# Performance work log

Measured on AMD Instinct MI355X. Metric: run time of the kernel, lower is better.

Reference implementation:

```python
import jax, jax.numpy as jnp
import numpy as np

N_NODES = 100000
N_EDGES = 1600000
D_FEAT = 128
HIDDEN = 128
N_CLASSES = 10
NUM_GRAPHS = 64


def setup_inputs() -> dict:
    key = jax.random.key(0)
    ks = jax.random.split(key, 12)
    x = jax.random.normal(ks[0], (N_NODES, D_FEAT), dtype=jnp.float32)
    edge_index = jax.random.randint(ks[1], (2, N_EDGES), 0, N_NODES, dtype=jnp.int32)
    batch = jnp.sort(jax.random.randint(ks[2], (N_NODES,), 0, NUM_GRAPHS, dtype=jnp.int32))
    s = 1.0 / np.sqrt(HIDDEN)
    def lin(k, out_d, in_d):
        return jax.random.uniform(k, (out_d, in_d), jnp.float32, -s, s)
    return {
        "x": x,
        "edge_index": edge_index,
        "batch": batch,
        "W1l": lin(ks[3], HIDDEN, D_FEAT), "b1": jnp.zeros((HIDDEN,), jnp.float32),
        "W1r": lin(ks[4], HIDDEN, D_FEAT),
        "W2l": lin(ks[5], HIDDEN, HIDDEN), "b2": jnp.zeros((HIDDEN,), jnp.float32),
        "W2r": lin(ks[6], HIDDEN, HIDDEN),
        "W3l": lin(ks[7], HIDDEN, HIDDEN), "b3": jnp.zeros((HIDDEN,), jnp.float32),
        "W3r": lin(ks[8], HIDDEN, HIDDEN),
        "Wout": lin(ks[9], N_CLASSES, HIDDEN), "bout": jnp.zeros((N_CLASSES,), jnp.float32),
    }


def reference(x, edge_index, batch, W1l, b1, W1r, W2l, b2, W2r, W3l, b3, W3r, Wout, bout):
    src, dst = edge_index[0], edge_index[1]
    n = x.shape[0]

    def sage(h, Wl, b, Wr):
        # sum-aggregate neighbor features: scatter-add x[src] into dst rows
        agg = jax.ops.segment_sum(h[src], dst, num_segments=n)  # [N, d]
        return agg @ Wl.T + b + h @ Wr.T

    h = jax.nn.relu(sage(x, W1l, b1, W1r))
    h = jax.nn.relu(sage(h, W2l, b2, W2r))
    h = sage(h, W3l, b3, W3r)
    pooled = jax.ops.segment_sum(h, batch, num_segments=NUM_GRAPHS)  # [G, hidden]
    # dropout is identity in eval mode
    return pooled @ Wout.T + bout
```

## Files before the change

kernel.cpp:

```cpp
#include <hip/hip_runtime.h>
#include <hip/hip_bf16.h>

#define N_NODES  100000
#define N_EDGES  1600000
#define D_FEAT   128
#define HIDDEN   128
#define N_CLASSES 10
#define NUM_GRAPHS 64

#define NBUCK 250
#define NPB   400
#define BCAP  7168
#define GT    64
#define NPAD  100096
#define NTILES (NPAD / GT)

typedef __bf16 bf16x8 __attribute__((ext_vector_type(8)));
typedef float  f32x4  __attribute__((ext_vector_type(4)));

static __device__ __forceinline__ unsigned short f2bf(float f) {
    __bf16 b = (__bf16)f;
    return __builtin_bit_cast(unsigned short, b);
}

static __device__ __forceinline__ void async_copy16(void* lds, const void* g) {
    __builtin_amdgcn_global_load_lds(
        (const __attribute__((address_space(1))) void*)g,
        (__attribute__((address_space(3))) void*)lds, 16, 0, 0);
}

__global__ void conv_w6_kernel(const float* __restrict__ W0, const float* __restrict__ W1,
                               const float* __restrict__ W2, const float* __restrict__ W3,
                               const float* __restrict__ W4, const float* __restrict__ W5,
                               __bf16* __restrict__ out) {
    const float* Ws[6] = {W0, W1, W2, W3, W4, W5};
    int m = blockIdx.x >> 6;
    int i = (blockIdx.x & 63) * 256 + threadIdx.x;
    out[m * (HIDDEN * D_FEAT) + i] = (__bf16)Ws[m][i];
}

__global__ __launch_bounds__(256) void xconv_kernel(const float* __restrict__ x,
                                                    __bf16* __restrict__ out) {
    int i = blockIdx.x * 256 + threadIdx.x;
    bf16x8 o;
    if (i < N_NODES * 128 / 8) {
        float4 v0 = ((const float4*)x)[i * 2];
        float4 v1 = ((const float4*)x)[i * 2 + 1];
        o[0] = (__bf16)v0.x; o[1] = (__bf16)v0.y; o[2] = (__bf16)v0.z; o[3] = (__bf16)v0.w;
        o[4] = (__bf16)v1.x; o[5] = (__bf16)v1.y; o[6] = (__bf16)v1.z; o[7] = (__bf16)v1.w;
    } else {
        #pragma unroll
        for (int k = 0; k < 8; k++) o[k] = (__bf16)0.f;
    }
    if (i < NPAD * 128 / 8) ((bf16x8*)out)[i] = o;
}

__global__ __launch_bounds__(256) void bucket_scatter_kernel(const int* __restrict__ ei,
                                                             int* __restrict__ gcur,
                                                             int2* __restrict__ bkt) {
    __shared__ int h[NBUCK];
    __shared__ int lb[NBUCK];
    int t = threadIdx.x;
    const int CH = N_EDGES / 256;
    for (int i = t; i < NBUCK; i += 256) h[i] = 0;
    __syncthreads();
    int e0 = blockIdx.x * CH;
    for (int e = e0 + t; e < e0 + CH; e += 256) {
        int d = ei[N_EDGES + e];
        atomicAdd(&h[d / NPB], 1);
    }
    __syncthreads();
    for (int i = t; i < NBUCK; i += 256) {
        lb[i] = atomicAdd(&gcur[i], h[i]);
        h[i] = 0;
    }
    __syncthreads();
    for (int e = e0 + t; e < e0 + CH; e += 256) {
        int s = ei[e];
        int d = ei[N_EDGES + e];
        int bb = d / NPB;
        int pos = lb[bb] + atomicAdd(&h[bb], 1);
        if (pos < BCAP) bkt[(size_t)bb * BCAP + pos] = make_int2(s, d);
    }
}

__global__ __launch_bounds__(256) void bucket_csr_kernel(const int2* __restrict__ bkt,
                                                         const int* __restrict__ gcur,
                                                         int2* __restrict__ rpse,
                                                         int* __restrict__ csr_src) {
    const int b = blockIdx.x;
    const int n0 = b * NPB;
    const int base = b * BCAP;
    int m = gcur[b]; if (m > BCAP) m = BCAP;
    __shared__ int cnt[NPB];
    __shared__ int part[128];
    __shared__ int excl[NPB];
    int t = threadIdx.x;
    for (int i = t; i < NPB; i += 256) cnt[i] = 0;
    __syncthreads();
    for (int e = t; e < m; e += 256) {
        int2 p = bkt[base + e];
        atomicAdd(&cnt[p.y - n0], 1);
    }
    __syncthreads();
    int gs = 0;
    if (t < 100) { gs = cnt[4 * t] + cnt[4 * t + 1] + cnt[4 * t + 2] + cnt[4 * t + 3]; part[t] = gs; }
    else if (t < 128) part[t] = 0;
    __syncthreads();
    for (int off = 1; off < 128; off <<= 1) {
        int x = 0;
        if (t < 128 && t >= off) x = part[t - off];
        __syncthreads();
        if (t < 128) part[t] += x;
        __syncthreads();
    }
    if (t < 100) part[t] -= gs;
    __syncthreads();
    for (int i = t; i < NPB; i += 256) {
        int g = i >> 2;
        int e0 = part[g];
        for (int j = g * 4; j < i; j++) e0 += cnt[j];
        excl[i] = e0;
    }
    __syncthreads();
    for (int i = t; i < NPB; i += 256) {
        rpse[n0 + i] = make_int2(base + excl[i], base + excl[i] + cnt[i]);
    }
    __syncthreads();
    for (int i = t; i < NPB; i += 256) cnt[i] = excl[i];
    __syncthreads();
    for (int e = t; e < m; e += 256) {
        int2 p = bkt[base + e];
        int pos = base + atomicAdd(&cnt[p.y - n0], 1);
        csr_src[pos] = p.x;
    }
}

__global__ __launch_bounds__(256) void gather_kernel(
    const __bf16* __restrict__ h, const int2* __restrict__ rpse,
    const int* __restrict__ csr_src, __bf16* __restrict__ agg, int N)
{
    int nid = blockIdx.x * 16 + (threadIdx.x >> 4);
    if (nid >= N) return;
    int f8 = threadIdx.x & 15;
    int2 se = rpse[nid];

    float a[8] = {0.f, 0.f, 0.f, 0.f, 0.f, 0.f, 0.f, 0.f};

    int j = se.x;
    for (; j + 3 < se.y; j += 4) {
        int s0 = csr_src[j];
        int s1 = csr_src[j + 1];
        int s2 = csr_src[j + 2];
        int s3 = csr_src[j + 3];
        bf16x8 u0 = ((const bf16x8*)h)[(size_t)s0 * 16 + f8];
        bf16x8 u1 = ((const bf16x8*)h)[(size_t)s1 * 16 + f8];
        bf16x8 u2 = ((const bf16x8*)h)[(size_t)s2 * 16 + f8];
        bf16x8 u3 = ((const bf16x8*)h)[(size_t)s3 * 16 + f8];
        #pragma unroll
        for (int i = 0; i < 8; i++)
            a[i] += ((float)u0[i] + (float)u1[i]) + ((float)u2[i] + (float)u3[i]);
    }
    for (; j < se.y; j++) {
        int s0 = csr_src[j];
        bf16x8 u0 = ((const bf16x8*)h)[(size_t)s0 * 16 + f8];
        #pragma unroll
        for (int i = 0; i < 8; i++) a[i] += (float)u0[i];
    }
    bf16x8 o;
    #pragma unroll
    for (int i = 0; i < 8; i++) o[i] = (__bf16)a[i];
    ((bf16x8*)agg)[(size_t)nid * 16 + f8] = o;
}

template<bool RELU>
__global__ __launch_bounds__(256) void fused_gemm_kernel(
    const __bf16* __restrict__ hA,
    const __bf16* __restrict__ hG,
    const __bf16* __restrict__ Wl, const __bf16* __restrict__ Wr,
    const float* __restrict__ bias,
    __bf16* __restrict__ outp, int M)
{
    __shared__ __bf16 lds[2][GT * 128];

    const int tid  = threadIdx.x;
    const int wave = tid >> 6;
    const int lane = tid & 63;
    const int kq = lane >> 4;
    const int ln = lane & 15;
    const int node_base = blockIdx.x * GT;
    const int f_base = wave * 32;

    {
        const __bf16* gsrc = hG + (size_t)node_base * 128;
        const __bf16* asrc = hA + (size_t)node_base * 128;
        #pragma unroll
        for (int i = 0; i < 4; i++) {
            int u = i * 256 + tid;
            int row = u >> 4;
            int sc = (u & 15) ^ (row & 15);
            async_copy16(&lds[0][u * 8], gsrc + row * 128 + sc * 8);
            async_copy16(&lds[1][u * 8], asrc + row * 128 + sc * 8);
        }
    }

    bf16x8 wfragL[2][4], wfragR[2][4];
    #pragma unroll
    for (int t = 0; t < 2; t++) {
        int wrow = f_base + t * 16 + ln;
        #pragma unroll
        for (int kc = 0; kc < 4; kc++) {
            int k0 = kc * 32 + kq * 8;
            wfragL[t][kc] = *(const bf16x8*)(Wl + wrow * 128 + k0);
            wfragR[t][kc] = *(const bf16x8*)(Wr + wrow * 128 + k0);
        }
    }
    float4 bias4[2];
    bias4[0] = *(const float4*)(bias + f_base + kq * 4);
    bias4[1] = *(const float4*)(bias + f_base + 16 + kq * 4);

    __syncthreads();

    #pragma unroll 2
    for (int tau = 0; tau < GT / 16; tau++) {
        int r = tau * 16 + ln;
        bf16x8 gfrag[4], afrag[4];
        #pragma unroll
        for (int kc = 0; kc < 4; kc++) {
            int c = (4 * kc + kq) ^ ln;
            gfrag[kc] = *(const bf16x8*)&lds[0][r * 128 + c * 8];
            afrag[kc] = *(const bf16x8*)&lds[1][r * 128 + c * 8];
        }

        f32x4 acc[2] = {(f32x4)(0.f), (f32x4)(0.f)};
        #pragma unroll
        for (int kc = 0; kc < 4; kc++) {
            #pragma unroll
            for (int t = 0; t < 2; t++) {
                acc[t] = __builtin_amdgcn_mfma_f32_16x16x32_bf16(wfragL[t][kc], gfrag[kc], acc[t], 0, 0, 0);
                acc[t] = __builtin_amdgcn_mfma_f32_16x16x32_bf16(wfragR[t][kc], afrag[kc], acc[t], 0, 0, 0);
            }
        }

        int node = node_base + tau * 16 + ln;
        if (node < M) {
            size_t rowoff = (size_t)node * 128;
            #pragma unroll
            for (int t = 0; t < 2; t++) {
                int fc = f_base + t * 16 + kq * 4;
                ushort4 o;
                float v0 = acc[t][0] + bias4[t].x;
                float v1 = acc[t][1] + bias4[t].y;
                float v2 = acc[t][2] + bias4[t].z;
                float v3 = acc[t][3] + bias4[t].w;
                if (RELU) {
                    v0 = fmaxf(v0, 0.f); v1 = fmaxf(v1, 0.f);
                    v2 = fmaxf(v2, 0.f); v3 = fmaxf(v3, 0.f);
                }
                o.x = f2bf(v0); o.y = f2bf(v1); o.z = f2bf(v2); o.w = f2bf(v3);
                *(ushort4*)(outp + rowoff + fc) = o;
            }
        }
    }
}

__global__ __launch_bounds__(256) void pool_kernel(
    const __bf16* __restrict__ h, const int* __restrict__ batch,
    float* __restrict__ pooled, int N)
{
    int idx = blockIdx.x * 256 + threadIdx.x;
    int f = idx & 127;
    int chunk = idx >> 7;
    int n0 = chunk * 32;
    if (n0 >= N) return;
    int n1 = n0 + 32; if (n1 > N) n1 = N;
    int curb = batch[n0];
    float acc = 0.f;
    for (int n = n0; n < n1; n++) {
        int b = batch[n];
        if (b != curb) {
            unsafeAtomicAdd(&pooled[(size_t)curb * 128 + f], acc);
            acc = 0.f; curb = b;
        }
        acc += (float)h[(size_t)n * 128 + f];
    }
    unsafeAtomicAdd(&pooled[(size_t)curb * 128 + f], acc);
}

__global__ void final_gemm_kernel(
    const float* __restrict__ pooled, const float* __restrict__ Wout,
    const float* __restrict__ bout, float* __restrict__ out)
{
    int idx = blockIdx.x * 64 + threadIdx.x;
    if (idx < NUM_GRAPHS * N_CLASSES) {
        int g = idx / N_CLASSES;
        int c = idx % N_CLASSES;
        float acc = bout[c];
        for (int k = 0; k < HIDDEN; k++)
            acc += pooled[g * HIDDEN + k] * Wout[c * HIDDEN + k];
        out[idx] = acc;
    }
}

extern "C" void kernel_launch(void* const* d_in, const int* in_sizes, int n_in,
                              void* d_out, int out_size, void* d_ws, size_t ws_size,
                              hipStream_t stream) {
    const float* x     = (const float*)d_in[0];
    const int*   ei    = (const int*)d_in[1];
    const int*   batch = (const int*)d_in[2];
    const float* W1l = (const float*)d_in[3];
    const float* b1  = (const float*)d_in[4];
    const float* W1r = (const float*)d_in[5];
    const float* W2l = (const float*)d_in[6];
    const float* b2  = (const float*)d_in[7];
    const float* W2r = (const float*)d_in[8];
    const float* W3l = (const float*)d_in[9];
    const float* b3  = (const float*)d_in[10];
    const float* W3r = (const float*)d_in[11];
    const float* Wout = (const float*)d_in[12];
    const float* bout = (const float*)d_in[13];
    float* out = (float*)d_out;

    char* ws = (char*)d_ws;
    size_t off = 0;
    const size_t NB = (size_t)NPAD * 128 * sizeof(__bf16);
    __bf16* B0    = (__bf16*)(ws + off); off += NB;
    __bf16* B1    = (__bf16*)(ws + off); off += NB;
    __bf16* B2    = (__bf16*)(ws + off); off += NB;
    float* pooled = (float*)(ws + off);  off += (size_t)NUM_GRAPHS * HIDDEN * sizeof(float);
    __bf16* wbf   = (__bf16*)(ws + off); off += 6 * (size_t)HIDDEN * D_FEAT * sizeof(__bf16);
    int2* rpse    = (int2*)(ws + off);   off += (size_t)N_NODES * sizeof(int2);
    int* csr_src  = (int*)(ws + off);    off += (size_t)NBUCK * BCAP * sizeof(int);
    int2* bkt     = (int2*)(ws + off);   off += (size_t)NBUCK * BCAP * sizeof(int2);
    int* gcur     = (int*)(ws + off);    off += (NBUCK + 8) * sizeof(int);

    const int WSZ = HIDDEN * D_FEAT;

    conv_w6_kernel<<<6 * 64, 256, 0, stream>>>(W1l, W1r, W2l, W2r, W3l, W3r, wbf);
    xconv_kernel<<<NPAD * 128 / (256 * 8), 256, 0, stream>>>(x, B0);

    hipMemsetAsync(gcur, 0, NBUCK * sizeof(int), stream);
    bucket_scatter_kernel<<<256, 256, 0, stream>>>(ei, gcur, bkt);
    bucket_csr_kernel<<<NBUCK, 256, 0, stream>>>(bkt, gcur, rpse, csr_src);

    const int gath_grid = (N_NODES + 15) / 16;

    gather_kernel<<<gath_grid, 256, 0, stream>>>(B0, rpse, csr_src, B1, N_NODES);
    fused_gemm_kernel<true><<<NTILES, 256, 0, stream>>>(B0, B1, wbf + 0 * WSZ, wbf + 1 * WSZ, b1, B2, N_NODES);

    gather_kernel<<<gath_grid, 256, 0, stream>>>(B2, rpse, csr_src, B1, N_NODES);
    fused_gemm_kernel<true><<<NTILES, 256, 0, stream>>>(B2, B1, wbf + 2 * WSZ, wbf + 3 * WSZ, b2, B0, N_NODES);

    gather_kernel<<<gath_grid, 256, 0, stream>>>(B0, rpse, csr_src, B1, N_NODES);
    fused_gemm_kernel<false><<<NTILES, 256, 0, stream>>>(B0, B1, wbf + 4 * WSZ, wbf + 5 * WSZ, b3, B2, N_NODES);

    hipMemsetAsync(pooled, 0, (size_t)NUM_GRAPHS * HIDDEN * sizeof(float), stream);
    const int pool_grid = ((N_NODES + 31) / 32 * 128 + 255) / 256;
    pool_kernel<<<pool_grid, 256, 0, stream>>>(B2, batch, pooled, N_NODES);
    final_gemm_kernel<<<10, 64, 0, stream>>>(pooled, Wout, bout, out);
}
```

Measured before the change: 439.7 us.

## Fuse last-layer GEMM with pooling, pack bucket entries, widen gather batching

```diff
diff --git a/kernel.cpp b/kernel.cpp
--- a/kernel.cpp
+++ b/kernel.cpp
@@ -57,11 +57,11 @@
 
 __global__ __launch_bounds__(256) void bucket_scatter_kernel(const int* __restrict__ ei,
                                                              int* __restrict__ gcur,
-                                                             int2* __restrict__ bkt) {
+                                                             int* __restrict__ bkt) {
     __shared__ int h[NBUCK];
     __shared__ int lb[NBUCK];
     int t = threadIdx.x;
-    const int CH = N_EDGES / 256;
+    const int CH = N_EDGES / 64;
     for (int i = t; i < NBUCK; i += 256) h[i] = 0;
     __syncthreads();
     int e0 = blockIdx.x * CH;
@@ -80,11 +80,11 @@
         int d = ei[N_EDGES + e];
         int bb = d / NPB;
         int pos = lb[bb] + atomicAdd(&h[bb], 1);
-        if (pos < BCAP) bkt[(size_t)bb * BCAP + pos] = make_int2(s, d);
-    }
-}
-
-__global__ __launch_bounds__(256) void bucket_csr_kernel(const int2* __restrict__ bkt,
+        if (pos < BCAP) bkt[(size_t)bb * BCAP + pos] = s | ((d - bb * NPB) << 17);
+    }
+}
+
+__global__ __launch_bounds__(256) void bucket_csr_kernel(const int* __restrict__ bkt,
                                                          const int* __restrict__ gcur,
                                                          int2* __restrict__ rpse,
                                                          int* __restrict__ csr_src) {
@@ -99,8 +99,8 @@
     for (int i = t; i < NPB; i += 256) cnt[i] = 0;
     __syncthreads();
     for (int e = t; e < m; e += 256) {
-        int2 p = bkt[base + e];
-        atomicAdd(&cnt[p.y - n0], 1);
+        int p = bkt[base + e];
+        atomicAdd(&cnt[p >> 17], 1);
     }
     __syncthreads();
     int gs = 0;
@@ -130,9 +130,9 @@
     for (int i = t; i < NPB; i += 256) cnt[i] = excl[i];
     __syncthreads();
     for (int e = t; e < m; e += 256) {
-        int2 p = bkt[base + e];
-        int pos = base + atomicAdd(&cnt[p.y - n0], 1);
-        csr_src[pos] = p.x;
+        int p = bkt[base + e];
+        int pos = base + atomicAdd(&cnt[p >> 17], 1);
+        csr_src[pos] = p & 131071;
     }
 }
 
@@ -144,28 +144,31 @@
     if (nid >= N) return;
     int f8 = threadIdx.x & 15;
     int2 se = rpse[nid];
+    int deg = se.y - se.x;
 
     float a[8] = {0.f, 0.f, 0.f, 0.f, 0.f, 0.f, 0.f, 0.f};
 
-    int j = se.x;
-    for (; j + 3 < se.y; j += 4) {
-        int s0 = csr_src[j];
-        int s1 = csr_src[j + 1];
-        int s2 = csr_src[j + 2];
-        int s3 = csr_src[j + 3];
-        bf16x8 u0 = ((const bf16x8*)h)[(size_t)s0 * 16 + f8];
-        bf16x8 u1 = ((const bf16x8*)h)[(size_t)s1 * 16 + f8];
-        bf16x8 u2 = ((const bf16x8*)h)[(size_t)s2 * 16 + f8];
-        bf16x8 u3 = ((const bf16x8*)h)[(size_t)s3 * 16 + f8];
-        #pragma unroll
-        for (int i = 0; i < 8; i++)
-            a[i] += ((float)u0[i] + (float)u1[i]) + ((float)u2[i] + (float)u3[i]);
-    }
-    for (; j < se.y; j++) {
-        int s0 = csr_src[j];
-        bf16x8 u0 = ((const bf16x8*)h)[(size_t)s0 * 16 + f8];
-        #pragma unroll
-        for (int i = 0; i < 8; i++) a[i] += (float)u0[i];
+    if (deg > 0) {
+        int iters = (deg + 7) >> 3;
+        int j = se.x;
+        #pragma unroll 1
+        for (int it = 0; it < iters; it++, j += 8) {
+            bf16x8 u[8];
+            float msk[8];
+            #pragma unroll
+            for (int i = 0; i < 8; i++) {
+                int jj = j + i;
+                int cl = jj < se.y ? jj : se.y - 1;
+                int s = csr_src[cl];
+                u[i] = ((const bf16x8*)h)[(size_t)s * 16 + f8];
+                msk[i] = (jj < se.y) ? 1.f : 0.f;
+            }
+            #pragma unroll
+            for (int i = 0; i < 8; i++) {
+                #pragma unroll
+                for (int k = 0; k < 8; k++) a[k] += msk[i] * (float)u[i][k];
+            }
+        }
     }
     bf16x8 o;
     #pragma unroll
@@ -175,8 +178,7 @@
 
 template<bool RELU>
 __global__ __launch_bounds__(256) void fused_gemm_kernel(
-    const __bf16* __restrict__ hA,
-    const __bf16* __restrict__ hG,
+    const __bf16* __restrict__ hA, const __bf16* __restrict__ hG,
     const __bf16* __restrict__ Wl, const __bf16* __restrict__ Wr,
     const float* __restrict__ bias,
     __bf16* __restrict__ outp, int M)
@@ -248,7 +250,6 @@
             #pragma unroll
             for (int t = 0; t < 2; t++) {
                 int fc = f_base + t * 16 + kq * 4;
-                ushort4 o;
                 float v0 = acc[t][0] + bias4[t].x;
                 float v1 = acc[t][1] + bias4[t].y;
                 float v2 = acc[t][2] + bias4[t].z;
@@ -257,6 +258,7 @@
                     v0 = fmaxf(v0, 0.f); v1 = fmaxf(v1, 0.f);
                     v2 = fmaxf(v2, 0.f); v3 = fmaxf(v3, 0.f);
                 }
+                ushort4 o;
                 o.x = f2bf(v0); o.y = f2bf(v1); o.z = f2bf(v2); o.w = f2bf(v3);
                 *(ushort4*)(outp + rowoff + fc) = o;
             }
@@ -264,27 +266,126 @@
     }
 }
 
-__global__ __launch_bounds__(256) void pool_kernel(
-    const __bf16* __restrict__ h, const int* __restrict__ batch,
-    float* __restrict__ pooled, int N)
+__global__ __launch_bounds__(256) void fused_gemm_pool_kernel(
+    const __bf16* __restrict__ hA, const __bf16* __restrict__ hG,
+    const __bf16* __restrict__ Wl, const __bf16* __restrict__ Wr,
+    const float* __restrict__ bias, const int* __restrict__ batch,
+    float* __restrict__ pooled, int M)
 {
-    int idx = blockIdx.x * 256 + threadIdx.x;
-    int f = idx & 127;
-    int chunk = idx >> 7;
-    int n0 = chunk * 32;
-    if (n0 >= N) return;
-    int n1 = n0 + 32; if (n1 > N) n1 = N;
-    int curb = batch[n0];
-    float acc = 0.f;
-    for (int n = n0; n < n1; n++) {
-        int b = batch[n];
-        if (b != curb) {
-            unsafeAtomicAdd(&pooled[(size_t)curb * 128 + f], acc);
-            acc = 0.f; curb = b;
-        }
-        acc += (float)h[(size_t)n * 128 + f];
-    }
-    unsafeAtomicAdd(&pooled[(size_t)curb * 128 + f], acc);
+    __shared__ __bf16 lds[2][GT * 128];
+
+    const int tid  = threadIdx.x;
+    const int wave = tid >> 6;
+    const int lane = tid & 63;
+    const int kq = lane >> 4;
+    const int ln = lane & 15;
+    const int node_base = blockIdx.x * GT;
+    const int f_base = wave * 32;
+
+    {
+        const __bf16* gsrc = hG + (size_t)node_base * 128;
+        const __bf16* asrc = hA + (size_t)node_base * 128;
+        #pragma unroll
+        for (int i = 0; i < 4; i++) {
+            int u = i * 256 + tid;
+            int row = u >> 4;
+            int sc = (u & 15) ^ (row & 15);
+            async_copy16(&lds[0][u * 8], gsrc + row * 128 + sc * 8);
+            async_copy16(&lds[1][u * 8], asrc + row * 128 + sc * 8);
+        }
+    }
+
+    bf16x8 wfragL[2][4], wfragR[2][4];
+    #pragma unroll
+    for (int t = 0; t < 2; t++) {
+        int wrow = f_base + t * 16 + ln;
+        #pragma unroll
+        for (int kc = 0; kc < 4; kc++) {
+            int k0 = kc * 32 + kq * 8;
+            wfragL[t][kc] = *(const bf16x8*)(Wl + wrow * 128 + k0);
+            wfragR[t][kc] = *(const bf16x8*)(Wr + wrow * 128 + k0);
+        }
+    }
+    float4 bias4[2];
+    bias4[0] = *(const float4*)(bias + f_base + kq * 4);
+    bias4[1] = *(const float4*)(bias + f_base + 16 + kq * 4);
+
+    int nb_cl = node_base < M ? node_base : (M - 1);
+    int ne_cl = node_base + GT - 1 < M ? node_base + GT - 1 : (M - 1);
+    int g0 = batch[nb_cl];
+    bool uniform = (batch[ne_cl] == g0) && (node_base + GT <= M);
+
+    float pacc[2][4] = {{0.f,0.f,0.f,0.f},{0.f,0.f,0.f,0.f}};
+
+    __syncthreads();
+
+    #pragma unroll 2
+    for (int tau = 0; tau < GT / 16; tau++) {
+        int r = tau * 16 + ln;
+        bf16x8 gfrag[4], afrag[4];
+        #pragma unroll
+        for (int kc = 0; kc < 4; kc++) {
+            int c = (4 * kc + kq) ^ ln;
+            gfrag[kc] = *(const bf16x8*)&lds[0][r * 128 + c * 8];
+            afrag[kc] = *(const bf16x8*)&lds[1][r * 128 + c * 8];
+        }
+
+        f32x4 acc[2] = {(f32x4)(0.f), (f32x4)(0.f)};
+        #pragma unroll
+        for (int kc = 0; kc < 4; kc++) {
+            #pragma unroll
+            for (int t = 0; t < 2; t++) {
+                acc[t] = __builtin_amdgcn_mfma_f32_16x16x32_bf16(wfragL[t][kc], gfrag[kc], acc[t], 0, 0, 0);
+                acc[t] = __builtin_amdgcn_mfma_f32_16x16x32_bf16(wfragR[t][kc], afrag[kc], acc[t], 0, 0, 0);
+            }
+        }
+
+        int node = node_base + tau * 16 + ln;
+        if (uniform) {
+            #pragma unroll
+            for (int t = 0; t < 2; t++) {
+                pacc[t][0] += acc[t][0] + bias4[t].x;
+                pacc[t][1] += acc[t][1] + bias4[t].y;
+                pacc[t][2] += acc[t][2] + bias4[t].z;
+                pacc[t][3] += acc[t][3] + bias4[t].w;
+            }
+        } else if (node < M) {
+            int g = batch[node];
+            #pragma unroll
+            for (int t = 0; t < 2; t++) {
+                int fc = f_base + t * 16 + kq * 4;
+                unsafeAtomicAdd(&pooled[g * 128 + fc + 0], acc[t][0] + bias4[t].x);
+                unsafeAtomicAdd(&pooled[g * 128 + fc + 1], acc[t][1] + bias4[t].y);
+                unsafeAtomicAdd(&pooled[g * 128 + fc + 2], acc[t][2] + bias4[t].z);
+                unsafeAtomicAdd(&pooled[g * 128 + fc + 3], acc[t][3] + bias4[t].w);
+            }
+        }
+    }
+
+    if (uniform) {
+        #pragma unroll
+        for (int t = 0; t < 2; t++) {
+            #pragma unroll
+            for (int i = 0; i < 4; i++) {
+                float v = pacc[t][i];
+                v += __shfl_xor(v, 1, 64);
+                v += __shfl_xor(v, 2, 64);
+                v += __shfl_xor(v, 4, 64);
+                v += __shfl_xor(v, 8, 64);
+                pacc[t][i] = v;
+            }
+        }
+        if (ln == 0) {
+            #pragma unroll
+            for (int t = 0; t < 2; t++) {
+                int fc = f_base + t * 16 + kq * 4;
+                unsafeAtomicAdd(&pooled[g0 * 128 + fc + 0], pacc[t][0]);
+                unsafeAtomicAdd(&pooled[g0 * 128 + fc + 1], pacc[t][1]);
+                unsafeAtomicAdd(&pooled[g0 * 128 + fc + 2], pacc[t][2]);
+                unsafeAtomicAdd(&pooled[g0 * 128 + fc + 3], pacc[t][3]);
+            }
+        }
+    }
 }
 
 __global__ void final_gemm_kernel(
@@ -331,7 +432,7 @@
     __bf16* wbf   = (__bf16*)(ws + off); off += 6 * (size_t)HIDDEN * D_FEAT * sizeof(__bf16);
     int2* rpse    = (int2*)(ws + off);   off += (size_t)N_NODES * sizeof(int2);
     int* csr_src  = (int*)(ws + off);    off += (size_t)NBUCK * BCAP * sizeof(int);
-    int2* bkt     = (int2*)(ws + off);   off += (size_t)NBUCK * BCAP * sizeof(int2);
+    int* bkt      = (int*)(ws + off);    off += (size_t)NBUCK * BCAP * sizeof(int);
     int* gcur     = (int*)(ws + off);    off += (NBUCK + 8) * sizeof(int);
 
     const int WSZ = HIDDEN * D_FEAT;
@@ -340,8 +441,9 @@
     xconv_kernel<<<NPAD * 128 / (256 * 8), 256, 0, stream>>>(x, B0);
 
     hipMemsetAsync(gcur, 0, NBUCK * sizeof(int), stream);
-    bucket_scatter_kernel<<<256, 256, 0, stream>>>(ei, gcur, bkt);
+    bucket_scatter_kernel<<<64, 256, 0, stream>>>(ei, gcur, bkt);
     bucket_csr_kernel<<<NBUCK, 256, 0, stream>>>(bkt, gcur, rpse, csr_src);
+    hipMemsetAsync(pooled, 0, (size_t)NUM_GRAPHS * HIDDEN * sizeof(float), stream);
 
     const int gath_grid = (N_NODES + 15) / 16;
 
@@ -352,10 +454,7 @@
     fused_gemm_kernel<true><<<NTILES, 256, 0, stream>>>(B2, B1, wbf + 2 * WSZ, wbf + 3 * WSZ, b2, B0, N_NODES);
 
     gather_kernel<<<gath_grid, 256, 0, stream>>>(B0, rpse, csr_src, B1, N_NODES);
-    fused_gemm_kernel<false><<<NTILES, 256, 0, stream>>>(B0, B1, wbf + 4 * WSZ, wbf + 5 * WSZ, b3, B2, N_NODES);
-
-    hipMemsetAsync(pooled, 0, (size_t)NUM_GRAPHS * HIDDEN * sizeof(float), stream);
-    const int pool_grid = ((N_NODES + 31) / 32 * 128 + 255) / 256;
-    pool_kernel<<<pool_grid, 256, 0, stream>>>(B2, batch, pooled, N_NODES);
+    fused_gemm_pool_kernel<<<NTILES, 256, 0, stream>>>(B0, B1, wbf + 4 * WSZ, wbf + 5 * WSZ, b3, batch, pooled, N_NODES);
+
     final_gemm_kernel<<<10, 64, 0, stream>>>(pooled, Wout, bout, out);
 }
```

After: 601.9 us. 36.9% more time.
